# Performance work log

Hardware: AMD Instinct MI355X
Metric: run time of the kernel (lower is better)

Reference implementation:

```python
import jax, jax.numpy as jnp
import numpy as np

B, L, H, HKV, D, HID, FFN = 32, 4096, 32, 2, 128, 4096, 13696
ROT = 64  # rotary_dim = kv_channels // 2 (GLM style)
EPS = 1e-5


def setup_inputs() -> dict:
    key = jax.random.key(0)
    ks = jax.random.split(key, 9)
    s = 0.02
    return {
        "hidden_states": jax.random.normal(ks[0], (B, HID), jnp.float32),
        "context_lens": jax.random.randint(ks[1], (B,), 1, L - 1, dtype=jnp.int32),
        "key_cache": jax.random.normal(ks[2], (B, L, HKV, D), jnp.float32),
        "value_cache": jax.random.normal(ks[3], (B, L, HKV, D), jnp.float32),
        "w_ln1": jnp.ones((HID,), jnp.float32),
        "w_ln2": jnp.ones((HID,), jnp.float32),
        "w_qkv": jax.random.normal(ks[4], (HID, H * D + 2 * HKV * D), jnp.float32) * s,
        "b_qkv": jax.random.normal(ks[5], (H * D + 2 * HKV * D,), jnp.float32) * s,
        "w_dense": jax.random.normal(ks[6], (H * D, HID), jnp.float32) * s,
        "w_h4h": jax.random.normal(ks[7], (HID, 2 * FFN), jnp.float32) * s,
        "w_4hh": jax.random.normal(ks[8], (FFN, HID), jnp.float32) * s,
    }


def rmsnorm(x, w):
    v = jnp.mean(x.astype(jnp.float32) ** 2, axis=-1, keepdims=True)
    return (w * (x * jax.lax.rsqrt(v + EPS))).astype(x.dtype)


def apply_rope(x, pos):
    # x: [B, heads, D]; GPT-J interleaved rotary on first ROT dims (glm=True)
    half = ROT // 2
    inv = 1.0 / (10000.0 ** (jnp.arange(half, dtype=jnp.float32) / half))
    f = pos.astype(jnp.float32)[:, None] * inv[None, :]          # [B, half]
    cos, sin = jnp.cos(f)[:, None, :], jnp.sin(f)[:, None, :]    # [B,1,half]
    xr, xp = x[..., :ROT], x[..., ROT:]
    x1, x2 = xr[..., 0::2], xr[..., 1::2]
    rot = jnp.stack([x1 * cos - x2 * sin, x2 * cos + x1 * sin], axis=-1).reshape(xr.shape)
    return jnp.concatenate([rot, xp], axis=-1)


def reference(hidden_states, context_lens, key_cache, value_cache,
              w_ln1, w_ln2, w_qkv, b_qkv, w_dense, w_h4h, w_4hh):
    # input RMSNorm
    ln1 = rmsnorm(hidden_states, w_ln1)
    # fused QKV projection (add_qkv_bias=True)
    qkv = ln1 @ w_qkv + b_qkv
    q, k, v = jnp.split(qkv, [H * D, H * D + HKV * D], axis=-1)
    q = apply_rope(q.reshape(B, H, D), context_lens)
    k = apply_rope(k.reshape(B, HKV, D), context_lens)
    v = v.reshape(B, HKV, D)
    # write new K/V into the paged cache at this token's slot
    kc = key_cache.at[jnp.arange(B), context_lens].set(k)
    vc = value_cache.at[jnp.arange(B), context_lens].set(v)
    # GQA attention: 32 q heads grouped over 2 kv heads
    qg = q.reshape(B, HKV, H // HKV, D)
    scores = jnp.einsum('bghd,blgd->bghl', qg, kc) * (D ** -0.5)
    mask = jnp.arange(L)[None, :] <= context_lens[:, None]       # [B, L]
    scores = jnp.where(mask[:, None, None, :], scores, -jnp.inf)
    p = jax.nn.softmax(scores, axis=-1)
    ctx = jnp.einsum('bghl,blgd->bghd', p, vc).reshape(B, H * D)
    attn_out = ctx @ w_dense                                     # add_bias_linear=False
    x = hidden_states + attn_out                                  # residual pre-LN
    ln2 = rmsnorm(x, w_ln2)
    g, u = jnp.split(ln2 @ w_h4h, 2, axis=-1)
    out = (jax.nn.silu(g) * u) @ w_4hh + x
    return out
```

## Files before the change

### kernel.cpp

```cpp
#include <hip/hip_runtime.h>
#include <hip/hip_bf16.h>

#define B_    32
#define L_    4096
#define H_    32
#define HKV_  2
#define GQ_   16
#define D_    128
#define HID_  4096
#define FFN_  13696
#define NQKV_ 4608
#define ROT_  64
#define EPS_  1e-5f

#define WAVE_POS_ 128
#define NSPLIT_   32

#define KS_QKV_  16
#define KS_DEN_  24
#define KS_H4H_  3
#define KS_4HH_  24

typedef __attribute__((ext_vector_type(8))) __bf16 bf16x8;
typedef __attribute__((ext_vector_type(4))) float  f32x4;

__device__ __forceinline__ void gl_lds16(const float* g, float* l) {
    __builtin_amdgcn_global_load_lds((const __attribute__((address_space(1))) void*)g,
                                     (__attribute__((address_space(3))) void*)l, 16, 0, 0);
}

__global__ __launch_bounds__(1024) void rmsnorm1_k(const float* __restrict__ x,
                                                   const float* __restrict__ w,
                                                   const float* __restrict__ bias,
                                                   __bf16* __restrict__ out,
                                                   float* __restrict__ qacc)
{
    int b = blockIdx.x;
    for (int i = threadIdx.x; i < NQKV_; i += 1024)
        qacc[(size_t)b * NQKV_ + i] = bias[i];
    const float* row = x + (size_t)b * HID_;
    float vals[4];
    float ss = 0.f;
#pragma unroll
    for (int i = 0; i < 4; ++i) {
        vals[i] = row[threadIdx.x + i * 1024];
        ss += vals[i] * vals[i];
    }
#pragma unroll
    for (int m = 1; m < 64; m <<= 1) ss += __shfl_xor(ss, m);
    __shared__ float wred[16];
    if ((threadIdx.x & 63) == 0) wred[threadIdx.x >> 6] = ss;
    __syncthreads();
    ss = 0.f;
#pragma unroll
    for (int wv = 0; wv < 16; ++wv) ss += wred[wv];
    float rs = rsqrtf(ss / HID_ + EPS_);
#pragma unroll
    for (int i = 0; i < 4; ++i) {
        int idx = threadIdx.x + i * 1024;
        out[(size_t)b * HID_ + idx] = (__bf16)(w[idx] * vals[i] * rs);
    }
}

template<int K, int N, int KSPLIT>
__global__ __launch_bounds__(256) void gemm16(const __bf16* __restrict__ A,
                                              const float* __restrict__ W,
                                              float* __restrict__ C)
{
    static_assert(K % 32 == 0, "K");
    constexpr int ksteps = K / 32;
    const int lane = threadIdx.x & 63;
    const int wid  = threadIdx.x >> 6;
    const int n0   = blockIdx.x * 128;
    const int cw   = wid * 32;
    const int r    = lane & 15;
    const int g4   = lane >> 4;
    const int s0   = (ksteps * (int)blockIdx.y) / KSPLIT;
    const int s1   = (ksteps * (int)(blockIdx.y + 1)) / KSPLIT;

    __shared__ float tiles[3][32][128];

    const int rhalf = lane >> 5;
    const int mslot = lane & 31;
    auto stage = [&](int s, float* dst) {
        if (s >= s1) return;
#pragma unroll
        for (int it = 0; it < 4; ++it) {
            int row  = wid * 8 + it * 2 + rhalf;
            int gcol = ((((mslot >> 1) ^ (row >> 3)) << 3) | ((mslot & 1) << 2));
            const float* src = W + (size_t)(s * 32 + row) * N + n0 + gcol;
            gl_lds16(src, dst + (size_t)(wid * 8 + it * 2) * 128);
        }
    };

    f32x4 acc00 = {0.f,0.f,0.f,0.f}, acc01 = acc00, acc10 = acc00, acc11 = acc00;
    const __bf16* a0p = A + (size_t)r * K;
    const __bf16* a1p = A + (size_t)(r + 16) * K;

    stage(s0,     &tiles[0][0][0]);
    stage(s0 + 1, &tiles[1][0][0]);

    const int c0 = cw + r, c1 = cw + r + 16;
    const int i0 = (((c0 >> 3) ^ g4) << 3) | (c0 & 7);
    const int i1 = (((c1 >> 3) ^ g4) << 3) | (c1 & 7);

    int bufc = 0;
    for (int s = s0; s < s1; ++s) {
        if (s + 1 < s1) asm volatile("s_waitcnt vmcnt(4)" ::: "memory");
        else            asm volatile("s_waitcnt vmcnt(0)" ::: "memory");
        __builtin_amdgcn_s_barrier();
        __builtin_amdgcn_sched_barrier(0);
        int bs = bufc + 2; if (bs >= 3) bs -= 3;
        stage(s + 2, &tiles[bs][0][0]);

        bf16x8 av0 = *(const bf16x8*)(a0p + s * 32 + g4 * 8);
        bf16x8 av1 = *(const bf16x8*)(a1p + s * 32 + g4 * 8);
        const float (*tile)[128] = tiles[bufc];
        bf16x8 b0f, b1f;
#pragma unroll
        for (int j = 0; j < 8; ++j) {
            b0f[j] = (__bf16)tile[g4 * 8 + j][i0];
            b1f[j] = (__bf16)tile[g4 * 8 + j][i1];
        }
        acc00 = __builtin_amdgcn_mfma_f32_16x16x32_bf16(av0, b0f, acc00, 0, 0, 0);
        acc10 = __builtin_amdgcn_mfma_f32_16x16x32_bf16(av1, b0f, acc10, 0, 0, 0);
        acc01 = __builtin_amdgcn_mfma_f32_16x16x32_bf16(av0, b1f, acc01, 0, 0, 0);
        acc11 = __builtin_amdgcn_mfma_f32_16x16x32_bf16(av1, b1f, acc11, 0, 0, 0);
        bufc = (bufc + 1 < 3) ? bufc + 1 : 0;
    }

    float* cp = C + n0 + cw;
#pragma unroll
    for (int i = 0; i < 4; ++i) {
        unsafeAtomicAdd(&cp[(size_t)(g4 * 4 + i) * N + r],           acc00[i]);
        unsafeAtomicAdd(&cp[(size_t)(g4 * 4 + i) * N + r + 16],      acc01[i]);
        unsafeAtomicAdd(&cp[(size_t)(16 + g4 * 4 + i) * N + r],      acc10[i]);
        unsafeAtomicAdd(&cp[(size_t)(16 + g4 * 4 + i) * N + r + 16], acc11[i]);
    }
}

__global__ __launch_bounds__(1024) void qkv_epi_k(const float* __restrict__ qacc,
                                                  const int* __restrict__ ctxl,
                                                  __bf16* __restrict__ qbf,
                                                  float* __restrict__ knew,
                                                  float* __restrict__ vnew)
{
    __shared__ float rowv[1152];
    __shared__ float cs[32], sn[32];
    int b = blockIdx.x, base = blockIdx.y * 1152;
    int pos = ctxl[b];
    if (threadIdx.x < 32) {
        int t = threadIdx.x;
        float inv = powf(10000.f, -(float)t * (1.0f / 32.0f));
        float f = (float)pos * inv;
        float sv, cv; sincosf(f, &sv, &cv);
        cs[t] = cv; sn[t] = sv;
    }
    for (int i0 = threadIdx.x; i0 < 1152; i0 += 1024)
        rowv[i0] = qacc[(size_t)b * NQKV_ + base + i0];
    __syncthreads();
    const float qscale = 0.08838834764831845f;
    for (int i0 = threadIdx.x; i0 < 1152; i0 += 1024) {
        int i = base + i0;
        int d = i & 127;
        if (i < HID_) {
            float o;
            if (d < ROT_) {
                int t = d >> 1;
                float cv = cs[t], sv = sn[t];
                float x1 = rowv[(i & ~1) - base], x2 = rowv[(i | 1) - base];
                o = (d & 1) ? (x2 * cv + x1 * sv) : (x1 * cv - x2 * sv);
            } else o = rowv[i0];
            qbf[(size_t)b * HID_ + i] = (__bf16)(o * qscale);
        } else {
            int j = i - HID_;
            if (j < HKV_ * D_) {
                float o;
                if (d < ROT_) {
                    int t = d >> 1;
                    float cv = cs[t], sv = sn[t];
                    float x1 = rowv[(i & ~1) - base], x2 = rowv[(i | 1) - base];
                    o = (d & 1) ? (x2 * cv + x1 * sv) : (x1 * cv - x2 * sv);
                } else o = rowv[i0];
                knew[(size_t)b * HKV_ * D_ + j] = o;
            } else {
                vnew[(size_t)b * HKV_ * D_ + (j - HKV_ * D_)] = rowv[i0];
            }
        }
    }
}

__global__ __launch_bounds__(256) void attn_k(const float* __restrict__ kc,
                                              const float* __restrict__ vc,
                                              const float* __restrict__ knew,
                                              const float* __restrict__ vnew,
                                              const __bf16* __restrict__ qbf,
                                              const int* __restrict__ ctxl,
                                              float* __restrict__ part)
{
    const int bg  = blockIdx.x;
    const int b   = bg >> 1, g = bg & 1;
    const int wid = threadIdx.x >> 6;
    const int split = blockIdx.y * 4 + wid;
    const int ctx = ctxl[b];
    const int p0  = split * WAVE_POS_;
    __shared__ __bf16 plds_all[4][16][40];
    if (p0 > ctx) return;
    const int pend = min(p0 + WAVE_POS_ - 1, ctx);
    const int lane = threadIdx.x & 63;
    const int r = lane & 15, g4 = lane >> 4;

    bf16x8 qf[4];
    {
        const __bf16* qp = qbf + (size_t)b * HID_ + (g * GQ_ + r) * D_ + g4 * 8;
#pragma unroll
        for (int kk = 0; kk < 4; ++kk) qf[kk] = *(const bf16x8*)(qp + kk * 32);
    }
    f32x4 acc[8];
#pragma unroll
    for (int dt = 0; dt < 8; ++dt) acc[dt] = (f32x4){0.f,0.f,0.f,0.f};
    float m_run[4], l_run[4];
#pragma unroll
    for (int i = 0; i < 4; ++i) { m_run[i] = -1e30f; l_run[i] = 0.f; }

    auto plds = plds_all[wid];
    const float* kbase = kc + ((size_t)b * L_ * HKV_ + g) * D_;
    const float* vbase = vc + ((size_t)b * L_ * HKV_ + g) * D_;
    const float* knp = knew + (size_t)(b * HKV_ + g) * D_;
    const float* vnp = vnew + (size_t)(b * HKV_ + g) * D_;

    for (int pc = p0; pc <= pend; pc += 32) {
        f32x4 sf[2];
#pragma unroll
        for (int pt = 0; pt < 2; ++pt) {
            int pos = pc + pt * 16 + r;
            const float* krow = (pos == ctx) ? knp : kbase + (size_t)pos * (HKV_ * D_);
            f32x4 s = {0.f,0.f,0.f,0.f};
#pragma unroll
            for (int kk = 0; kk < 4; ++kk) {
                const float4* kp = (const float4*)(krow + kk * 32 + g4 * 8);
                float4 fa = kp[0], fb = kp[1];
                bf16x8 kf = { (__bf16)fa.x, (__bf16)fa.y, (__bf16)fa.z, (__bf16)fa.w,
                              (__bf16)fb.x, (__bf16)fb.y, (__bf16)fb.z, (__bf16)fb.w };
                s = __builtin_amdgcn_mfma_f32_16x16x32_bf16(qf[kk], kf, s, 0, 0, 0);
            }
            sf[pt] = s;
        }
#pragma unroll
        for (int pt = 0; pt < 2; ++pt) {
            int pos = pc + pt * 16 + r;
            if (pos > ctx) {
#pragma unroll
                for (int i = 0; i < 4; ++i) sf[pt][i] = -1e30f;
            }
        }
#pragma unroll
        for (int i = 0; i < 4; ++i) {
            float mv = fmaxf(sf[0][i], sf[1][i]);
            mv = fmaxf(mv, __shfl_xor(mv, 1));
            mv = fmaxf(mv, __shfl_xor(mv, 2));
            mv = fmaxf(mv, __shfl_xor(mv, 4));
            mv = fmaxf(mv, __shfl_xor(mv, 8));
            float mnew = fmaxf(m_run[i], mv);
            float sc = __expf(m_run[i] - mnew);
            l_run[i] *= sc;
            m_run[i] = mnew;
#pragma unroll
            for (int dt = 0; dt < 8; ++dt) acc[dt][i] *= sc;
        }
#pragma unroll
        for (int pt = 0; pt < 2; ++pt) {
#pragma unroll
            for (int i = 0; i < 4; ++i) {
                float e = __expf(sf[pt][i] - m_run[i]);
                l_run[i] += e;
                plds[g4 * 4 + i][pt * 16 + r] = (__bf16)e;
            }
        }
        asm volatile("s_waitcnt lgkmcnt(0)" ::: "memory");
        __builtin_amdgcn_sched_barrier(0);
        bf16x8 pa = *(const bf16x8*)&plds[r][g4 * 8];
        const float* vrows[8];
#pragma unroll
        for (int j = 0; j < 8; ++j) {
            int pos = pc + g4 * 8 + j;
            vrows[j] = (pos == ctx) ? vnp : vbase + (size_t)pos * (HKV_ * D_);
        }
#pragma unroll
        for (int dt = 0; dt < 8; ++dt) {
            bf16x8 vf;
#pragma unroll
            for (int j = 0; j < 8; ++j) vf[j] = (__bf16)vrows[j][dt * 16 + r];
            acc[dt] = __builtin_amdgcn_mfma_f32_16x16x32_bf16(pa, vf, acc[dt], 0, 0, 0);
        }
        asm volatile("s_waitcnt lgkmcnt(0)" ::: "memory");
        __builtin_amdgcn_sched_barrier(0);
    }
#pragma unroll
    for (int i = 0; i < 4; ++i) {
        float lv = l_run[i];
        lv += __shfl_xor(lv, 1);
        lv += __shfl_xor(lv, 2);
        lv += __shfl_xor(lv, 4);
        lv += __shfl_xor(lv, 8);
        l_run[i] = lv;
    }
    float* pb = part + ((size_t)bg * NSPLIT_ + split) * 16 * 130;
#pragma unroll
    for (int dt = 0; dt < 8; ++dt)
#pragma unroll
        for (int i = 0; i < 4; ++i)
            pb[(g4 * 4 + i) * 130 + dt * 16 + r] = acc[dt][i];
    if (r == 0) {
#pragma unroll
        for (int i = 0; i < 4; ++i) {
            pb[(g4 * 4 + i) * 130 + 128] = m_run[i];
            pb[(g4 * 4 + i) * 130 + 129] = l_run[i];
        }
    }
}

__global__ __launch_bounds__(1024) void attn_comb_k(const float* __restrict__ part,
                                                    const int* __restrict__ ctxl,
                                                    const float* __restrict__ hidden,
                                                    __bf16* __restrict__ ctxb,
                                                    float* __restrict__ dacc)
{
    int bg = blockIdx.x;
    int c  = blockIdx.y;
    int b = bg >> 1, g = bg & 1;
    {
        int seg = (g * 2 + c) * 1024 + threadIdx.x;
        dacc[(size_t)b * HID_ + seg] = hidden[(size_t)b * HID_ + seg];
    }
    int ctx = ctxl[b];
    int ns = ctx / WAVE_POS_ + 1;
    const float* pb = part + (size_t)bg * NSPLIT_ * 16 * 130;
    __shared__ float mlm[NSPLIT_][16], wgt[NSPLIT_][16];
    __shared__ float Mh[16], Ih[16];
    int t = threadIdx.x;
    if (t < NSPLIT_ * 16) {
        int s = t >> 4, h = t & 15;
        mlm[s][h] = pb[(s * 16 + h) * 130 + 128];
        wgt[s][h] = pb[(s * 16 + h) * 130 + 129];
    }
    __syncthreads();
    if (t < 16) {
        int h = t;
        float M = -1e30f;
        for (int s = 0; s < ns; ++s) M = fmaxf(M, mlm[s][h]);
        float den = 0.f;
        for (int s = 0; s < ns; ++s) den += __expf(mlm[s][h] - M) * wgt[s][h];
        Mh[h] = M; Ih[h] = 1.f / den;
    }
    __syncthreads();
    if (t < NSPLIT_ * 16) {
        int s = t >> 4, h = t & 15;
        wgt[s][h] = __expf(mlm[s][h] - Mh[h]) * Ih[h];
    }
    __syncthreads();
    int h = t >> 6, dd = (t & 63) + c * 64;
    float o = 0.f;
    for (int s = 0; s < ns; ++s)
        o += wgt[s][h] * pb[(s * 16 + h) * 130 + dd];
    ctxb[(size_t)b * HID_ + (g * GQ_ + h) * D_ + dd] = (__bf16)o;
}

__global__ __launch_bounds__(1024) void dense_red_k(const float* __restrict__ dacc,
                                                    float* __restrict__ xout,
                                                    float* __restrict__ outbuf,
                                                    float* __restrict__ ssq)
{
    int b = blockIdx.x;
    int i = blockIdx.y * 1024 + threadIdx.x;
    float v = dacc[(size_t)b * HID_ + i];
    xout[(size_t)b * HID_ + i] = v;
    outbuf[(size_t)b * HID_ + i] = v;
    float ss = v * v;
#pragma unroll
    for (int m = 1; m < 64; m <<= 1) ss += __shfl_xor(ss, m);
    __shared__ float wred[16];
    if ((threadIdx.x & 63) == 0) wred[threadIdx.x >> 6] = ss;
    __syncthreads();
    if (threadIdx.x == 0) {
        float s = 0.f;
#pragma unroll
        for (int wv = 0; wv < 16; ++wv) s += wred[wv];
        ssq[b * 4 + blockIdx.y] = s;
    }
}

__global__ __launch_bounds__(1024) void rms2_k(const float* __restrict__ xbuf,
                                               const float* __restrict__ ssq,
                                               const float* __restrict__ wln2,
                                               __bf16* __restrict__ a2,
                                               float* __restrict__ guacc)
{
    int b = blockIdx.x;
    for (int i = threadIdx.x; i < 2 * FFN_; i += 1024)
        guacc[(size_t)b * 2 * FFN_ + i] = 0.f;
    float ss = ssq[b * 4] + ssq[b * 4 + 1] + ssq[b * 4 + 2] + ssq[b * 4 + 3];
    float rs = rsqrtf(ss / HID_ + EPS_);
#pragma unroll
    for (int it = 0; it < 4; ++it) {
        int i = threadIdx.x + it * 1024;
        a2[(size_t)b * HID_ + i] = (__bf16)(wln2[i] * xbuf[(size_t)b * HID_ + i] * rs);
    }
}

__global__ __launch_bounds__(256) void act_k(const float* __restrict__ guacc,
                                             __bf16* __restrict__ act)
{
    int i = blockIdx.x * 256 + threadIdx.x;
    int b = blockIdx.y;
    if (i < FFN_) {
        const float* gp = guacc + (size_t)b * 2 * FFN_;
        float gv = gp[i];
        float uv = gp[FFN_ + i];
        float s = gv / (1.f + __expf(-gv));
        act[(size_t)b * FFN_ + i] = (__bf16)(s * uv);
    }
}

extern "C" void kernel_launch(void* const* d_in, const int* in_sizes, int n_in,
                              void* d_out, int out_size, void* d_ws, size_t ws_size,
                              hipStream_t stream)
{
    const float* hidden  = (const float*)d_in[0];
    const int*   ctxl    = (const int*)d_in[1];
    const float* kcache  = (const float*)d_in[2];
    const float* vcache  = (const float*)d_in[3];
    const float* w_ln1   = (const float*)d_in[4];
    const float* w_ln2   = (const float*)d_in[5];
    const float* w_qkv   = (const float*)d_in[6];
    const float* b_qkv   = (const float*)d_in[7];
    const float* w_dense = (const float*)d_in[8];
    const float* w_h4h   = (const float*)d_in[9];
    const float* w_4hh   = (const float*)d_in[10];
    float* out = (float*)d_out;

    char* ws = (char*)d_ws;
    size_t off = 0;
    auto alloc = [&](size_t bytes) -> void* {
        void* p = ws + off;
        off += (bytes + 255) & ~(size_t)255;
        return p;
    };
    __bf16* a0    = (__bf16*)alloc((size_t)B_ * HID_ * 2);
    float*  qacc  = (float*) alloc((size_t)B_ * NQKV_ * 4);
    __bf16* qbf   = (__bf16*)alloc((size_t)B_ * HID_ * 2);
    float*  knew  = (float*) alloc((size_t)B_ * HKV_ * D_ * 4);
    float*  vnew  = (float*) alloc((size_t)B_ * HKV_ * D_ * 4);
    float*  apart = (float*) alloc((size_t)B_ * HKV_ * NSPLIT_ * 16 * 130 * 4);
    __bf16* ctxb  = (__bf16*)alloc((size_t)B_ * HID_ * 2);
    float*  dacc  = (float*) alloc((size_t)B_ * HID_ * 4);
    float*  xbuf  = (float*) alloc((size_t)B_ * HID_ * 4);
    float*  ssq   = (float*) alloc((size_t)B_ * 4 * 4);
    __bf16* a2    = (__bf16*)alloc((size_t)B_ * HID_ * 2);
    float*  guacc = (float*) alloc((size_t)B_ * 2 * FFN_ * 4);
    __bf16* actb  = (__bf16*)alloc((size_t)B_ * FFN_ * 2);
    (void)ws_size; (void)in_sizes; (void)n_in; (void)out_size;

    hipLaunchKernelGGL(rmsnorm1_k, dim3(B_), dim3(1024), 0, stream, hidden, w_ln1, b_qkv, a0, qacc);
    hipLaunchKernelGGL((gemm16<HID_, NQKV_, KS_QKV_>), dim3(NQKV_ / 128, KS_QKV_), dim3(256), 0, stream, a0, w_qkv, qacc);
    hipLaunchKernelGGL(qkv_epi_k, dim3(B_, 4), dim3(1024), 0, stream, qacc, ctxl, qbf, knew, vnew);
    hipLaunchKernelGGL(attn_k, dim3(B_ * HKV_, NSPLIT_ / 4), dim3(256), 0, stream,
                       kcache, vcache, knew, vnew, qbf, ctxl, apart);
    hipLaunchKernelGGL(attn_comb_k, dim3(B_ * HKV_, 2), dim3(1024), 0, stream, apart, ctxl, hidden, ctxb, dacc);
    hipLaunchKernelGGL((gemm16<HID_, HID_, KS_DEN_>), dim3(HID_ / 128, KS_DEN_), dim3(256), 0, stream, ctxb, w_dense, dacc);
    hipLaunchKernelGGL(dense_red_k, dim3(B_, 4), dim3(1024), 0, stream, dacc, xbuf, out, ssq);
    hipLaunchKernelGGL(rms2_k, dim3(B_), dim3(1024), 0, stream, xbuf, ssq, w_ln2, a2, guacc);
    hipLaunchKernelGGL((gemm16<HID_, 2 * FFN_, KS_H4H_>), dim3(2 * FFN_ / 128, KS_H4H_), dim3(256), 0, stream, a2, w_h4h, guacc);
    hipLaunchKernelGGL(act_k, dim3((FFN_ + 255) / 256, B_), dim3(256), 0, stream, guacc, actb);
    hipLaunchKernelGGL((gemm16<FFN_, HID_, KS_4HH_>), dim3(HID_ / 128, KS_4HH_), dim3(256), 0, stream, actb, w_4hh, out);
}
```

Baseline: 261.9 us.

## Fuse SiLU-gate into down-proj GEMM, prefetch A operand, widen small kernel grids

The separate activation kernel is removed: the down-projection GEMM now loads fp32 gate/up values directly, applies SiLU·up in registers, and converts to bf16, with the A-operand loads software-pipelined alongside the LDS weight stages. The xbuf copy is dropped by reading the residual from the output buffer. Bias init, rms2 and attention-combine kernels are split over more blocks so they use more CUs. This saves one launch and an activation round trip, at the cost of reading twice as many fp32 bytes for A and extra registers in the fused GEMM.

Measured after the change: 285.8 us. +9.1%, slower.

```diff
diff --git a/kernel.cpp b/kernel.cpp
--- a/kernel.cpp
+++ b/kernel.cpp
@@ -36,8 +36,12 @@
                                                    float* __restrict__ qacc)
 {
     int b = blockIdx.x;
-    for (int i = threadIdx.x; i < NQKV_; i += 1024)
-        qacc[(size_t)b * NQKV_ + i] = bias[i];
+    if (blockIdx.y > 0) {
+        int base = (blockIdx.y - 1) * 1152;
+        for (int i = threadIdx.x; i < 1152; i += 1024)
+            qacc[(size_t)b * NQKV_ + base + i] = bias[base + i];
+        return;
+    }
     const float* row = x + (size_t)b * HID_;
     float vals[4];
     float ss = 0.f;
@@ -62,8 +66,8 @@
     }
 }
 
-template<int K, int N, int KSPLIT>
-__global__ __launch_bounds__(256) void gemm16(const __bf16* __restrict__ A,
+template<int K, int N, int KSPLIT, int FUSE>
+__global__ __launch_bounds__(256) void gemm16(const void* __restrict__ Ap,
                                               const float* __restrict__ W,
                                               float* __restrict__ C)
 {
@@ -83,7 +87,6 @@
     const int rhalf = lane >> 5;
     const int mslot = lane & 31;
     auto stage = [&](int s, float* dst) {
-        if (s >= s1) return;
 #pragma unroll
         for (int it = 0; it < 4; ++it) {
             int row  = wid * 8 + it * 2 + rhalf;
@@ -93,12 +96,50 @@
         }
     };
 
+    const __bf16* a0p = (const __bf16*)Ap + (size_t)r * K;
+    const __bf16* a1p = (const __bf16*)Ap + (size_t)(r + 16) * K;
+    const float*  gu0 = (const float*)Ap + (size_t)r * (2 * K);
+    const float*  gu1 = (const float*)Ap + (size_t)(r + 16) * (2 * K);
+
+    bf16x8 avc0{}, avc1{}, avn0{}, avn1{};
+    float4 fc0[4], fc1[4], fn0[4], fn1[4];
+
+    auto issueA = [&](int s, bf16x8& b0, bf16x8& b1, float4* f0, float4* f1) {
+        int k0 = s * 32 + g4 * 8;
+        if constexpr (FUSE) {
+            f0[0] = *(const float4*)(gu0 + k0);
+            f0[1] = *(const float4*)(gu0 + k0 + 4);
+            f0[2] = *(const float4*)(gu0 + K + k0);
+            f0[3] = *(const float4*)(gu0 + K + k0 + 4);
+            f1[0] = *(const float4*)(gu1 + k0);
+            f1[1] = *(const float4*)(gu1 + k0 + 4);
+            f1[2] = *(const float4*)(gu1 + K + k0);
+            f1[3] = *(const float4*)(gu1 + K + k0 + 4);
+        } else {
+            b0 = *(const bf16x8*)(a0p + k0);
+            b1 = *(const bf16x8*)(a1p + k0);
+        }
+    };
+    auto cvtA = [&](const float4* f) -> bf16x8 {
+        bf16x8 o;
+        float gv[8] = {f[0].x, f[0].y, f[0].z, f[0].w, f[1].x, f[1].y, f[1].z, f[1].w};
+        float uv[8] = {f[2].x, f[2].y, f[2].z, f[2].w, f[3].x, f[3].y, f[3].z, f[3].w};
+#pragma unroll
+        for (int j = 0; j < 8; ++j) {
+            float s = gv[j] / (1.f + __expf(-gv[j]));
+            o[j] = (__bf16)(s * uv[j]);
+        }
+        return o;
+    };
+
     f32x4 acc00 = {0.f,0.f,0.f,0.f}, acc01 = acc00, acc10 = acc00, acc11 = acc00;
-    const __bf16* a0p = A + (size_t)r * K;
-    const __bf16* a1p = A + (size_t)(r + 16) * K;
-
-    stage(s0,     &tiles[0][0][0]);
-    stage(s0 + 1, &tiles[1][0][0]);
+
+    issueA(s0, avc0, avc1, fc0, fc1);
+    stage(s0, &tiles[0][0][0]);
+    if (s0 + 1 < s1) {
+        issueA(s0 + 1, avn0, avn1, fn0, fn1);
+        stage(s0 + 1, &tiles[1][0][0]);
+    }
 
     const int c0 = cw + r, c1 = cw + r + 16;
     const int i0 = (((c0 >> 3) ^ g4) << 3) | (c0 & 7);
@@ -106,15 +147,25 @@
 
     int bufc = 0;
     for (int s = s0; s < s1; ++s) {
-        if (s + 1 < s1) asm volatile("s_waitcnt vmcnt(4)" ::: "memory");
-        else            asm volatile("s_waitcnt vmcnt(0)" ::: "memory");
+        if (s + 1 < s1) {
+            if constexpr (FUSE) asm volatile("s_waitcnt vmcnt(12)" ::: "memory");
+            else                asm volatile("s_waitcnt vmcnt(6)" ::: "memory");
+        } else {
+            asm volatile("s_waitcnt vmcnt(0)" ::: "memory");
+        }
         __builtin_amdgcn_s_barrier();
         __builtin_amdgcn_sched_barrier(0);
         int bs = bufc + 2; if (bs >= 3) bs -= 3;
-        stage(s + 2, &tiles[bs][0][0]);
-
-        bf16x8 av0 = *(const bf16x8*)(a0p + s * 32 + g4 * 8);
-        bf16x8 av1 = *(const bf16x8*)(a1p + s * 32 + g4 * 8);
+        bf16x8 t0{}, t1{};
+        float4 g0[4], g1[4];
+        if (s + 2 < s1) {
+            issueA(s + 2, t0, t1, g0, g1);
+            stage(s + 2, &tiles[bs][0][0]);
+        }
+
+        bf16x8 av0, av1;
+        if constexpr (FUSE) { av0 = cvtA(fc0); av1 = cvtA(fc1); }
+        else                { av0 = avc0;      av1 = avc1; }
         const float (*tile)[128] = tiles[bufc];
         bf16x8 b0f, b1f;
 #pragma unroll
@@ -126,6 +177,13 @@
         acc10 = __builtin_amdgcn_mfma_f32_16x16x32_bf16(av1, b0f, acc10, 0, 0, 0);
         acc01 = __builtin_amdgcn_mfma_f32_16x16x32_bf16(av0, b1f, acc01, 0, 0, 0);
         acc11 = __builtin_amdgcn_mfma_f32_16x16x32_bf16(av1, b1f, acc11, 0, 0, 0);
+
+        if constexpr (FUSE) {
+#pragma unroll
+            for (int q = 0; q < 4; ++q) { fc0[q] = fn0[q]; fc1[q] = fn1[q]; fn0[q] = g0[q]; fn1[q] = g1[q]; }
+        } else {
+            avc0 = avn0; avc1 = avn1; avn0 = t0; avn1 = t1;
+        }
         bufc = (bufc + 1 < 3) ? bufc + 1 : 0;
     }
 
@@ -320,17 +378,17 @@
     }
 }
 
-__global__ __launch_bounds__(1024) void attn_comb_k(const float* __restrict__ part,
-                                                    const int* __restrict__ ctxl,
-                                                    const float* __restrict__ hidden,
-                                                    __bf16* __restrict__ ctxb,
-                                                    float* __restrict__ dacc)
+__global__ __launch_bounds__(512) void attn_comb_k(const float* __restrict__ part,
+                                                   const int* __restrict__ ctxl,
+                                                   const float* __restrict__ hidden,
+                                                   __bf16* __restrict__ ctxb,
+                                                   float* __restrict__ dacc)
 {
     int bg = blockIdx.x;
     int c  = blockIdx.y;
     int b = bg >> 1, g = bg & 1;
     {
-        int seg = (g * 2 + c) * 1024 + threadIdx.x;
+        int seg = (g * 4 + c) * 512 + threadIdx.x;
         dacc[(size_t)b * HID_ + seg] = hidden[(size_t)b * HID_ + seg];
     }
     int ctx = ctxl[b];
@@ -339,7 +397,7 @@
     __shared__ float mlm[NSPLIT_][16], wgt[NSPLIT_][16];
     __shared__ float Mh[16], Ih[16];
     int t = threadIdx.x;
-    if (t < NSPLIT_ * 16) {
+    {
         int s = t >> 4, h = t & 15;
         mlm[s][h] = pb[(s * 16 + h) * 130 + 128];
         wgt[s][h] = pb[(s * 16 + h) * 130 + 129];
@@ -354,12 +412,12 @@
         Mh[h] = M; Ih[h] = 1.f / den;
     }
     __syncthreads();
-    if (t < NSPLIT_ * 16) {
+    {
         int s = t >> 4, h = t & 15;
         wgt[s][h] = __expf(mlm[s][h] - Mh[h]) * Ih[h];
     }
     __syncthreads();
-    int h = t >> 6, dd = (t & 63) + c * 64;
+    int h = t >> 5, dd = (t & 31) + c * 32;
     float o = 0.f;
     for (int s = 0; s < ns; ++s)
         o += wgt[s][h] * pb[(s * 16 + h) * 130 + dd];
@@ -367,14 +425,12 @@
 }
 
 __global__ __launch_bounds__(1024) void dense_red_k(const float* __restrict__ dacc,
-                                                    float* __restrict__ xout,
                                                     float* __restrict__ outbuf,
                                                     float* __restrict__ ssq)
 {
     int b = blockIdx.x;
     int i = blockIdx.y * 1024 + threadIdx.x;
     float v = dacc[(size_t)b * HID_ + i];
-    xout[(size_t)b * HID_ + i] = v;
     outbuf[(size_t)b * HID_ + i] = v;
     float ss = v * v;
 #pragma unroll
@@ -390,35 +446,20 @@
     }
 }
 
-__global__ __launch_bounds__(1024) void rms2_k(const float* __restrict__ xbuf,
+__global__ __launch_bounds__(1024) void rms2_k(const float* __restrict__ xb,
                                                const float* __restrict__ ssq,
                                                const float* __restrict__ wln2,
                                                __bf16* __restrict__ a2,
                                                float* __restrict__ guacc)
 {
-    int b = blockIdx.x;
-    for (int i = threadIdx.x; i < 2 * FFN_; i += 1024)
-        guacc[(size_t)b * 2 * FFN_ + i] = 0.f;
+    int b = blockIdx.x, y = blockIdx.y;
+    for (int i = threadIdx.x; i < 3424; i += 1024)
+        guacc[(size_t)b * 2 * FFN_ + y * 3424 + i] = 0.f;
     float ss = ssq[b * 4] + ssq[b * 4 + 1] + ssq[b * 4 + 2] + ssq[b * 4 + 3];
     float rs = rsqrtf(ss / HID_ + EPS_);
-#pragma unroll
-    for (int it = 0; it < 4; ++it) {
-        int i = threadIdx.x + it * 1024;
-        a2[(size_t)b * HID_ + i] = (__bf16)(wln2[i] * xbuf[(size_t)b * HID_ + i] * rs);
-    }
-}
-
-__global__ __launch_bounds__(256) void act_k(const float* __restrict__ guacc,
-                                             __bf16* __restrict__ act)
-{
-    int i = blockIdx.x * 256 + threadIdx.x;
-    int b = blockIdx.y;
-    if (i < FFN_) {
-        const float* gp = guacc + (size_t)b * 2 * FFN_;
-        float gv = gp[i];
-        float uv = gp[FFN_ + i];
-        float s = gv / (1.f + __expf(-gv));
-        act[(size_t)b * FFN_ + i] = (__bf16)(s * uv);
+    if (threadIdx.x < 512) {
+        int i = y * 512 + threadIdx.x;
+        a2[(size_t)b * HID_ + i] = (__bf16)(wln2[i] * xb[(size_t)b * HID_ + i] * rs);
     }
 }
 
@@ -454,23 +495,20 @@
     float*  apart = (float*) alloc((size_t)B_ * HKV_ * NSPLIT_ * 16 * 130 * 4);
     __bf16* ctxb  = (__bf16*)alloc((size_t)B_ * HID_ * 2);
     float*  dacc  = (float*) alloc((size_t)B_ * HID_ * 4);
-    float*  xbuf  = (float*) alloc((size_t)B_ * HID_ * 4);
     float*  ssq   = (float*) alloc((size_t)B_ * 4 * 4);
     __bf16* a2    = (__bf16*)alloc((size_t)B_ * HID_ * 2);
     float*  guacc = (float*) alloc((size_t)B_ * 2 * FFN_ * 4);
-    __bf16* actb  = (__bf16*)alloc((size_t)B_ * FFN_ * 2);
     (void)ws_size; (void)in_sizes; (void)n_in; (void)out_size;
 
-    hipLaunchKernelGGL(rmsnorm1_k, dim3(B_), dim3(1024), 0, stream, hidden, w_ln1, b_qkv, a0, qacc);
-    hipLaunchKernelGGL((gemm16<HID_, NQKV_, KS_QKV_>), dim3(NQKV_ / 128, KS_QKV_), dim3(256), 0, stream, a0, w_qkv, qacc);
+    hipLaunchKernelGGL(rmsnorm1_k, dim3(B_, 5), dim3(1024), 0, stream, hidden, w_ln1, b_qkv, a0, qacc);
+    hipLaunchKernelGGL((gemm16<HID_, NQKV_, KS_QKV_, 0>), dim3(NQKV_ / 128, KS_QKV_), dim3(256), 0, stream, a0, w_qkv, qacc);
     hipLaunchKernelGGL(qkv_epi_k, dim3(B_, 4), dim3(1024), 0, stream, qacc, ctxl, qbf, knew, vnew);
     hipLaunchKernelGGL(attn_k, dim3(B_ * HKV_, NSPLIT_ / 4), dim3(256), 0, stream,
                        kcache, vcache, knew, vnew, qbf, ctxl, apart);
-    hipLaunchKernelGGL(attn_comb_k, dim3(B_ * HKV_, 2), dim3(1024), 0, stream, apart, ctxl, hidden, ctxb, dacc);
-    hipLaunchKernelGGL((gemm16<HID_, HID_, KS_DEN_>), dim3(HID_ / 128, KS_DEN_), dim3(256), 0, stream, ctxb, w_dense, dacc);
-    hipLaunchKernelGGL(dense_red_k, dim3(B_, 4), dim3(1024), 0, stream, dacc, xbuf, out, ssq);
-    hipLaunchKernelGGL(rms2_k, dim3(B_), dim3(1024), 0, stream, xbuf, ssq, w_ln2, a2, guacc);
-    hipLaunchKernelGGL((gemm16<HID_, 2 * FFN_, KS_H4H_>), dim3(2 * FFN_ / 128, KS_H4H_), dim3(256), 0, stream, a2, w_h4h, guacc);
-    hipLaunchKernelGGL(act_k, dim3((FFN_ + 255) / 256, B_), dim3(256), 0, stream, guacc, actb);
-    hipLaunchKernelGGL((gemm16<FFN_, HID_, KS_4HH_>), dim3(HID_ / 128, KS_4HH_), dim3(256), 0, stream, actb, w_4hh, out);
-}
+    hipLaunchKernelGGL(attn_comb_k, dim3(B_ * HKV_, 4), dim3(512), 0, stream, apart, ctxl, hidden, ctxb, dacc);
+    hipLaunchKernelGGL((gemm16<HID_, HID_, KS_DEN_, 0>), dim3(HID_ / 128, KS_DEN_), dim3(256), 0, stream, ctxb, w_dense, dacc);
+    hipLaunchKernelGGL(dense_red_k, dim3(B_, 4), dim3(1024), 0, stream, dacc, out, ssq);
+    hipLaunchKernelGGL(rms2_k, dim3(B_, 8), dim3(1024), 0, stream, out, ssq, w_ln2, a2, guacc);
+    hipLaunchKernelGGL((gemm16<HID_, 2 * FFN_, KS_H4H_, 0>), dim3(2 * FFN_ / 128, KS_H4H_), dim3(256), 0, stream, a2, w_h4h, guacc);
+    hipLaunchKernelGGL((gemm16<FFN_, HID_, KS_4HH_, 1>), dim3(HID_ / 128, KS_4HH_), dim3(256), 0, stream, guacc, w_4hh, out);
+}
```
